# Kernel tuning notes

Measured on AMD Instinct MI355X. Metric: run time of the kernel, lower is better.

## Reference

```python
import jax, jax.numpy as jnp
import numpy as np
from jax import lax

H = 8       # heads == channel dim for conv projections
D = 64      # base_dim (per-head width)
B = 8
N = 1024
EPS = 1e-5  # BatchNorm eps (torch default)


def _bn2d(y, g, b, m, v):
    # inference-mode BatchNorm2d over channel axis 1
    inv = g / jnp.sqrt(v + EPS)
    return (y - m[None, :, None, None]) * inv[None, :, None, None] + b[None, :, None, None]


def _sepconv(xh, dw, dwb, g, bb, m, v, pw, pwb):
    # xh: [b, H, n, d] treated as NCHW; depthwise 3x3 (groups=H) + BN + pointwise 1x1
    y = lax.conv_general_dilated(xh, dw, window_strides=(1, 1),
                                 padding=((1, 1), (1, 1)),
                                 feature_group_count=H,
                                 dimension_numbers=('NCHW', 'OIHW', 'NCHW'))
    y = y + dwb[None, :, None, None]
    y = _bn2d(y, g, bb, m, v)
    # pointwise 1x1 conv == channel mix
    y = jnp.einsum('oc,bchw->bohw', pw[:, :, 0, 0], y) + pwb[None, :, None, None]
    return y


def setup_inputs() -> dict:
    key = jax.random.key(0)
    ks = jax.random.split(key, 12)
    s = 0.1
    x = jax.random.normal(ks[0], (B, N, H * D), jnp.float32)
    dw_w = jax.random.normal(ks[1], (3, H, 1, 3, 3), jnp.float32) * s
    dw_b = jax.random.normal(ks[2], (3, H), jnp.float32) * s
    bn_g = 1.0 + 0.1 * jax.random.normal(ks[3], (3, H), jnp.float32)
    bn_b = jax.random.normal(ks[4], (3, H), jnp.float32) * s
    bn_m = jnp.zeros((3, H), jnp.float32)
    bn_v = jnp.ones((3, H), jnp.float32)
    pw_w = jax.random.normal(ks[5], (3, H, H, 1, 1), jnp.float32) * s
    pw_b = jax.random.normal(ks[6], (3, H), jnp.float32) * s
    re_w = jax.random.normal(ks[7], (H, H, 1, 1), jnp.float32) * 0.3
    re_b = jax.random.normal(ks[8], (H,), jnp.float32) * s
    vn_g = 1.0 + 0.1 * jax.random.normal(ks[9], (H,), jnp.float32)
    vn_b = jax.random.normal(ks[10], (H,), jnp.float32) * s
    vn_m = jnp.zeros((H,), jnp.float32)
    vn_v = jnp.ones((H,), jnp.float32)
    out_w = jax.random.normal(ks[11], (H * D, H * D), jnp.float32) * 0.02
    out_b = jnp.zeros((H * D,), jnp.float32)
    return {"x": x, "dw_w": dw_w, "dw_b": dw_b, "bn_g": bn_g, "bn_b": bn_b,
            "bn_m": bn_m, "bn_v": bn_v, "pw_w": pw_w, "pw_b": pw_b,
            "re_w": re_w, "re_b": re_b, "vn_g": vn_g, "vn_b": vn_b,
            "vn_m": vn_m, "vn_v": vn_v, "out_w": out_w, "out_b": out_b}


def reference(x, dw_w, dw_b, bn_g, bn_b, bn_m, bn_v, pw_w, pw_b,
              re_w, re_b, vn_g, vn_b, vn_m, vn_v, out_w, out_b):
    b, n, hd = x.shape
    d = hd // H
    xh = x.reshape(b, n, H, d).transpose(0, 2, 1, 3)  # [b, h, n, d]
    q, k, v = [
        _sepconv(xh, dw_w[i], dw_b[i], bn_g[i], bn_b[i], bn_m[i], bn_v[i],
                 pw_w[i], pw_b[i])
        for i in range(3)
    ]
    scale = H ** -0.5  # note: original uses dim=heads for scale
    dots = jnp.einsum('bhid,bhjd->bhij', q, k) * scale  # [b,h,n,n]
    attn = jax.nn.softmax(dots, axis=-1)
    # re-attention: 1x1 cross-head conv + BatchNorm (reatten_scale = 1.0)
    attn = jnp.einsum('oc,bcij->boij', re_w[:, :, 0, 0], attn) + re_b[None, :, None, None]
    attn = _bn2d(attn, vn_g, vn_b, vn_m, vn_v)
    out = jnp.einsum('bhij,bhjd->bhid', attn, v)
    out = out.transpose(0, 2, 1, 3).reshape(b, n, hd)
    return out @ out_w.T + out_b
```

## Files before the change

### kernel.cpp

```cpp
#include <hip/hip_runtime.h>


#define EPS 1e-5f
#define SCALE 0.35355339059327373f

typedef float f32x4 __attribute__((ext_vector_type(4)));
typedef short short8 __attribute__((ext_vector_type(8)));
typedef unsigned short ushort;

#define MFMA16(a, b, c) __builtin_amdgcn_mfma_f32_16x16x32_bf16(a, b, c, 0, 0, 0)

__device__ __forceinline__ unsigned short f2bf(float f) {
  union { float f; unsigned u; } v; v.f = f;
  return (unsigned short)((v.u + 0x7FFFu + ((v.u >> 16) & 1u)) >> 16);
}
__device__ __forceinline__ float bf2f(unsigned short h) {
  union { unsigned u; float f; } v; v.u = ((unsigned)h) << 16;
  return v.f;
}
__device__ __forceinline__ int cvtpk(float lo, float hi) {
  int r;
  asm("v_cvt_pk_bf16_f32 %0, %1, %2" : "=v"(r) : "v"(lo), "v"(hi));
  return r;
}

__global__ __launch_bounds__(256) void kprep(
    const float* __restrict__ dwb, const float* __restrict__ bng,
    const float* __restrict__ bnb, const float* __restrict__ bnm,
    const float* __restrict__ bnv, const float* __restrict__ pww,
    const float* __restrict__ pwb, const float* __restrict__ rew,
    const float* __restrict__ reb, const float* __restrict__ vng,
    const float* __restrict__ vnb, const float* __restrict__ vnm,
    const float* __restrict__ vnv, const float* __restrict__ outw,
    float* __restrict__ smalls, float* __restrict__ vsum,
    ushort* __restrict__ wh, ushort* __restrict__ wl) {
  int g = blockIdx.x * 256 + threadIdx.x;
  if (g < 262144) {
    float v = outw[g];
    ushort hi = f2bf(v);
    wh[g] = hi;
    wl[g] = f2bf(v - bf2f(hi));
  }
  if (blockIdx.x >= 1 && blockIdx.x <= 16)
    vsum[(blockIdx.x - 1) * 256 + threadIdx.x] = 0.f;
  if (blockIdx.x == 0) {
    int t = threadIdx.x;
    if (t < 64) {
      int o = t >> 3, c = t & 7;
      float s = vng[o] * rsqrtf(vnv[o] + EPS);
      smalls[t] = rew[o * 8 + c] * s;
    }
    if (t < 8) {
      float s = vng[t] * rsqrtf(vnv[t] + EPS);
      smalls[64 + t] = (reb[t] - vnm[t]) * s + vnb[t];
    }
    if (t < 192) {
      int p = t >> 6, rem = t & 63, o = rem >> 3, c = rem & 7;
      float s = bng[p * 8 + c] * rsqrtf(bnv[p * 8 + c] + EPS);
      smalls[72 + t] = pww[(p * 8 + o) * 8 + c] * s;
    }
    if (t < 24) {
      int p = t / 8, o = t & 7;
      float acc = pwb[p * 8 + o];
      for (int c = 0; c < 8; ++c) {
        float s = bng[p * 8 + c] * rsqrtf(bnv[p * 8 + c] + EPS);
        acc += pww[(p * 8 + o) * 8 + c] *
               ((dwb[p * 8 + c] - bnm[p * 8 + c]) * s + bnb[p * 8 + c]);
      }
      smalls[264 + t] = acc;
    }
  }
}

__global__ __launch_bounds__(256) void kqkv(
    const float* __restrict__ x, const float* __restrict__ dww,
    const float* __restrict__ smalls,
    ushort* __restrict__ qb, ushort* __restrict__ kb,
    float* __restrict__ vf) {
  int t = threadIdx.x;
  int blk = blockIdx.x;
  int b = blk >> 8;
  int n0 = (blk & 255) << 2;
  int d = t & 63;
  int n = n0 + (t >> 6);
  const float* pw_eff = smalls + 72;
  const float* pwb_eff = smalls + 264;
  float y[3][8];
  for (int h = 0; h < 8; ++h) {
    float nb[3][3];
#pragma unroll
    for (int ky = 0; ky < 3; ++ky) {
      int nn = n - 1 + ky;
      bool vr = (nn >= 0) && (nn < 1024);
      const float* xp = x + ((b * 1024 + nn) * 512 + h * 64 + d);
      nb[ky][0] = (vr && d > 0) ? xp[-1] : 0.f;
      nb[ky][1] = vr ? xp[0] : 0.f;
      nb[ky][2] = (vr && d < 63) ? xp[1] : 0.f;
    }
#pragma unroll
    for (int p = 0; p < 3; ++p) {
      const float* w = dww + (p * 8 + h) * 9;
      float a = 0.f;
#pragma unroll
      for (int ky = 0; ky < 3; ++ky)
#pragma unroll
        for (int kx = 0; kx < 3; ++kx) a += w[ky * 3 + kx] * nb[ky][kx];
      y[p][h] = a;
    }
  }
#pragma unroll
  for (int p = 0; p < 3; ++p) {
#pragma unroll
    for (int o = 0; o < 8; ++o) {
      float a = pwb_eff[p * 8 + o];
#pragma unroll
      for (int c = 0; c < 8; ++c) a += pw_eff[p * 64 + o * 8 + c] * y[p][c];
      int idx = ((b * 8 + o) * 1024 + n) * 64 + d;
      if (p == 0) qb[idx] = f2bf(a * SCALE);
      else if (p == 1) kb[idx] = f2bf(a);
      else vf[idx] = a;
    }
  }
}

__global__ __launch_bounds__(256) void kvtrans(const float* __restrict__ vf,
                                               ushort* __restrict__ vt,
                                               float* __restrict__ vsum) {
  __shared__ ushort lds[64 * 65];
  __shared__ float red[256];
  int bh = blockIdx.x >> 4;
  int nt = blockIdx.x & 15;
  int t = threadIdx.x;
  const float* src = vf + (bh * 1024 + nt * 64) * 64;
  float part = 0.f;
#pragma unroll
  for (int it = 0; it < 16; ++it) {
    int nn = (t >> 6) + it * 4;
    int d = t & 63;
    float v = src[nn * 64 + d];
    part += v;
    lds[nn * 65 + d] = f2bf(v);
  }
  red[t] = part;
  __syncthreads();
  ushort* dst = vt + bh * 64 * 1024 + nt * 64;
#pragma unroll
  for (int it = 0; it < 16; ++it) {
    int d = (t >> 6) + it * 4;
    int n = t & 63;
    dst[d * 1024 + n] = lds[n * 65 + d];
  }
  if (t < 64)
    atomicAdd(&vsum[bh * 64 + t],
              red[t] + red[64 + t] + red[128 + t] + red[192 + t]);
}

__global__ __launch_bounds__(512, 4) void kattn(
    const ushort* __restrict__ qb, const ushort* __restrict__ kb,
    const ushort* __restrict__ vt, const float* __restrict__ smalls,
    const float* __restrict__ vsum,
    ushort* __restrict__ ohi, ushort* __restrict__ olo) {
  __shared__ ushort plds[16 * 512];
  __shared__ ushort mlds[8 * 1024];
  int b = blockIdx.x & 7;
  int it = blockIdx.x >> 3;
  int i0 = it * 16;
  int tid = threadIdx.x;
  int w = tid >> 6;
  int l = tid & 63;
  int lrow = l & 15, lgrp = l >> 4;

  const ushort* qh = qb + ((b * 8 + w) * 1024 + i0) * 64;
  const ushort* kh = kb + (b * 8 + w) * 1024 * 64;
  const ushort* vth = vt + (b * 8 + w) * 64 * 1024;

  short8 Qf[2];
#pragma unroll
  for (int kc = 0; kc < 2; ++kc)
    Qf[kc] = *(const short8*)(qh + lrow * 64 + kc * 32 + lgrp * 8);

  int ip = w + ((l >> 5) << 3);
  int jp = (l & 31) << 1;
  int s0 = w >> 2;
  bool s1 = (l >> 5) & 1;

  float Wc[64];
#pragma unroll
  for (int z = 0; z < 64; ++z) {
    int idx = z ^ (s0 << 1);
    Wc[z] = __builtin_bit_cast(
        float, __builtin_amdgcn_readfirstlane(
                   __builtin_bit_cast(int, smalls[idx])));
  }

  float rs[4] = {0.f, 0.f, 0.f, 0.f};
  for (int jt = 0; jt < 16; ++jt) {
    const ushort* kbase = kh + jt * 64 * 64;
    f32x4 acc[4] = {};
#pragma unroll
    for (int q = 0; q < 4; ++q)
#pragma unroll
      for (int kc = 0; kc < 2; ++kc) {
        short8 Kf = *(const short8*)(kbase + (q * 16 + lrow) * 64 + kc * 32 + lgrp * 8);
        acc[q] = MFMA16(Qf[kc], Kf, acc[q]);
      }
#pragma unroll
    for (int q = 0; q < 4; ++q)
#pragma unroll
      for (int r = 0; r < 4; ++r) rs[r] += __expf(acc[q][r]);
  }
#pragma unroll
  for (int r = 0; r < 4; ++r) {
    float v = rs[r];
    v += __shfl_xor(v, 1);
    v += __shfl_xor(v, 2);
    v += __shfl_xor(v, 4);
    v += __shfl_xor(v, 8);
    rs[r] = 1.f / v;
  }

  f32x4 Oacc[4] = {};
  for (int jt = 0; jt < 16; ++jt) {
    const ushort* kbase = kh + jt * 64 * 64;
    f32x4 acc[4] = {};
#pragma unroll
    for (int q = 0; q < 4; ++q)
#pragma unroll
      for (int kc = 0; kc < 2; ++kc) {
        short8 Kf = *(const short8*)(kbase + (q * 16 + lrow) * 64 + kc * 32 + lgrp * 8);
        acc[q] = MFMA16(Qf[kc], Kf, acc[q]);
      }
#pragma unroll
    for (int q = 0; q < 4; ++q)
#pragma unroll
      for (int r = 0; r < 4; ++r) {
        float p = __expf(acc[q][r]) * rs[r];
        int pi = (((lgrp * 4 + r) << 9) + ((q * 16 + lrow) << 3) + w) ^ (lgrp << 1);
        plds[pi] = (ushort)cvtpk(p, p);
      }
    __syncthreads();
    int pbase = (ip << 9) + (jp << 3);
    int4 r0 = *(const int4*)&plds[pbase];
    int4 r1 = *(const int4*)&plds[pbase + 8];
    int e0[4], e1[4];
    e0[0] = s1 ? r0.z : r0.x;  e0[1] = s1 ? r0.w : r0.y;
    e0[2] = s1 ? r0.x : r0.z;  e0[3] = s1 ? r0.y : r0.w;
    e1[0] = s1 ? r1.z : r1.x;  e1[1] = s1 ? r1.w : r1.y;
    e1[2] = s1 ? r1.x : r1.z;  e1[3] = s1 ? r1.y : r1.w;
    float o0[8] = {}, o1[8] = {};
#pragma unroll
    for (int m = 0; m < 4; ++m) {
      float p0l = __builtin_bit_cast(float, e0[m] << 16);
      float p0h = __builtin_bit_cast(float, (unsigned)e0[m] & 0xffff0000u);
      float p1l = __builtin_bit_cast(float, e1[m] << 16);
      float p1h = __builtin_bit_cast(float, (unsigned)e1[m] & 0xffff0000u);
#pragma unroll
      for (int o = 0; o < 8; ++o) {
        o0[o] += Wc[o * 8 + 2 * m] * p0l + Wc[o * 8 + 2 * m + 1] * p0h;
        o1[o] += Wc[o * 8 + 2 * m] * p1l + Wc[o * 8 + 2 * m + 1] * p1h;
      }
    }
#pragma unroll
    for (int o = 0; o < 8; ++o) {
      int pk = cvtpk(o0[o], o1[o]);
      int mi = ((o << 10) + (ip << 6) + jp) ^ ((ip & 7) << 3);
      *(int*)&mlds[mi] = pk;
    }
    __syncthreads();
    short8 PA[2];
#pragma unroll
    for (int kc = 0; kc < 2; ++kc) {
      int ai = ((w << 10) + (lrow << 6) + kc * 32 + lgrp * 8) ^ ((lrow & 7) << 3);
      PA[kc] = *(const short8*)&mlds[ai];
    }
#pragma unroll
    for (int nq = 0; nq < 4; ++nq)
#pragma unroll
      for (int kc = 0; kc < 2; ++kc) {
        short8 Vf = *(const short8*)(vth + (nq * 16 + lrow) * 1024 + jt * 64 + kc * 32 + lgrp * 8);
        Oacc[nq] = MFMA16(PA[kc], Vf, Oacc[nq]);
      }
  }

  float beta = smalls[64 + w];
#pragma unroll
  for (int nq = 0; nq < 4; ++nq)
#pragma unroll
    for (int r = 0; r < 4; ++r) {
      int i = i0 + lgrp * 4 + r;
      int dd = nq * 16 + lrow;
      float o = Oacc[nq][r] + beta * vsum[(b * 8 + w) * 64 + dd];
      int idx = (b * 1024 + i) * 512 + w * 64 + dd;
      ushort hi = (ushort)cvtpk(o, o);
      ohi[idx] = hi;
      olo[idx] = f2bf(o - bf2f(hi));
    }
}

__global__ __launch_bounds__(256) void kout(
    const ushort* __restrict__ ohi, const ushort* __restrict__ olo,
    const ushort* __restrict__ wh, const ushort* __restrict__ wl,
    const float* __restrict__ outb, float* __restrict__ out) {
  int w = threadIdx.x >> 6, l = threadIdx.x & 63;
  int lrow = l & 15, lgrp = l >> 4;
  int i0 = blockIdx.x * 128 + w * 32;
  int n0 = blockIdx.y * 64;
  f32x4 acc[2][4] = {};
  for (int kc = 0; kc < 16; ++kc) {
    short8 Ah[2], Al[2], Bh[4], Bl[4];
#pragma unroll
    for (int a = 0; a < 2; ++a) {
      int ro = (i0 + a * 16 + lrow) * 512 + kc * 32 + lgrp * 8;
      Ah[a] = *(const short8*)(ohi + ro);
      Al[a] = *(const short8*)(olo + ro);
    }
#pragma unroll
    for (int nq = 0; nq < 4; ++nq) {
      int ro = (n0 + nq * 16 + lrow) * 512 + kc * 32 + lgrp * 8;
      Bh[nq] = *(const short8*)(wh + ro);
      Bl[nq] = *(const short8*)(wl + ro);
    }
#pragma unroll
    for (int a = 0; a < 2; ++a)
#pragma unroll
      for (int nq = 0; nq < 4; ++nq) {
        acc[a][nq] = MFMA16(Ah[a], Bh[nq], acc[a][nq]);
        acc[a][nq] = MFMA16(Ah[a], Bl[nq], acc[a][nq]);
        acc[a][nq] = MFMA16(Al[a], Bh[nq], acc[a][nq]);
      }
  }
#pragma unroll
  for (int a = 0; a < 2; ++a)
#pragma unroll
    for (int nq = 0; nq < 4; ++nq)
#pragma unroll
      for (int r = 0; r < 4; ++r) {
        int row = i0 + a * 16 + lgrp * 4 + r;
        int n = n0 + nq * 16 + lrow;
        out[row * 512 + n] = acc[a][nq][r] + outb[n];
      }
}

extern "C" void kernel_launch(void* const* d_in, const int* in_sizes, int n_in,
                              void* d_out, int out_size, void* d_ws, size_t ws_size,
                              hipStream_t stream) {
  const float* x   = (const float*)d_in[0];
  const float* dww = (const float*)d_in[1];
  const float* dwb = (const float*)d_in[2];
  const float* bng = (const float*)d_in[3];
  const float* bnb = (const float*)d_in[4];
  const float* bnm = (const float*)d_in[5];
  const float* bnv = (const float*)d_in[6];
  const float* pww = (const float*)d_in[7];
  const float* pwb = (const float*)d_in[8];
  const float* rew = (const float*)d_in[9];
  const float* reb = (const float*)d_in[10];
  const float* vng = (const float*)d_in[11];
  const float* vnb = (const float*)d_in[12];
  const float* vnm = (const float*)d_in[13];
  const float* vnv = (const float*)d_in[14];
  const float* outw = (const float*)d_in[15];
  const float* outb = (const float*)d_in[16];

  char* ws = (char*)d_ws;
  const size_t MB = 1024 * 1024;
  ushort* qb  = (ushort*)(ws);
  ushort* kb  = (ushort*)(ws + 8 * MB);
  ushort* vt  = (ushort*)(ws + 16 * MB);
  float*  vf  = (float*)(ws + 24 * MB);
  ushort* ohi = (ushort*)(ws + 40 * MB);
  ushort* olo = (ushort*)(ws + 48 * MB);
  ushort* wh  = (ushort*)(ws + 56 * MB);
  ushort* wl  = (ushort*)(ws + 56 * MB + 512 * 1024);
  float* smalls = (float*)(ws + 57 * MB);
  float* vsum   = (float*)(ws + 57 * MB + 4096);

  hipLaunchKernelGGL(kprep, dim3(1024), dim3(256), 0, stream,
                     dwb, bng, bnb, bnm, bnv, pww, pwb, rew, reb, vng, vnb,
                     vnm, vnv, outw, smalls, vsum, wh, wl);
  hipLaunchKernelGGL(kqkv, dim3(2048), dim3(256), 0, stream,
                     x, dww, smalls, qb, kb, vf);
  hipLaunchKernelGGL(kvtrans, dim3(1024), dim3(256), 0, stream, vf, vt, vsum);
  hipLaunchKernelGGL(kattn, dim3(512), dim3(512), 0, stream,
                     qb, kb, vt, smalls, vsum, ohi, olo);
  hipLaunchKernelGGL(kout, dim3(64, 8), dim3(256), 0, stream,
                     ohi, olo, wh, wl, outb, (float*)d_out);
}
```

Before: 349.2 us.

## Split softmax row-sum into separate kernel and restructure attention across heads

Moves the softmax denominator pass out of the attention kernel into a new kernel that accumulates row sums of exp2 scores into a global buffer with atomics. Q is prescaled by log2(e) so exp2 can be used. The attention kernel now has each wave handle a slice of keys for all 8 heads, so the cross-head 1x1 mix happens in registers, and the per-wave partial outputs are reduced through shared memory. V is stored as bf16 instead of fp32 before the transpose. Together these remove the duplicated QK^T pass and the two-phase shared-memory shuffle, at the cost of an extra kernel launch, global atomics and a larger per-thread accumulator footprint (8x4 accumulators).

New measurement: 349.3 us. No clear change (+0.0%).

```diff
diff --git a/kernel.cpp b/kernel.cpp
--- a/kernel.cpp
+++ b/kernel.cpp
@@ -2,7 +2,7 @@
 
 
 #define EPS 1e-5f
-#define SCALE 0.35355339059327373f
+#define SCALE2 0.510138584f
 
 typedef float f32x4 __attribute__((ext_vector_type(4)));
 typedef short short8 __attribute__((ext_vector_type(8)));
@@ -33,7 +33,8 @@
     const float* __restrict__ vnb, const float* __restrict__ vnm,
     const float* __restrict__ vnv, const float* __restrict__ outw,
     float* __restrict__ smalls, float* __restrict__ vsum,
-    ushort* __restrict__ wh, ushort* __restrict__ wl) {
+    float* __restrict__ lsum, ushort* __restrict__ wh,
+    ushort* __restrict__ wl) {
   int g = blockIdx.x * 256 + threadIdx.x;
   if (g < 262144) {
     float v = outw[g];
@@ -43,6 +44,8 @@
   }
   if (blockIdx.x >= 1 && blockIdx.x <= 16)
     vsum[(blockIdx.x - 1) * 256 + threadIdx.x] = 0.f;
+  if (blockIdx.x >= 17 && blockIdx.x <= 272)
+    lsum[(blockIdx.x - 17) * 256 + threadIdx.x] = 0.f;
   if (blockIdx.x == 0) {
     int t = threadIdx.x;
     if (t < 64) {
@@ -76,7 +79,7 @@
     const float* __restrict__ x, const float* __restrict__ dww,
     const float* __restrict__ smalls,
     ushort* __restrict__ qb, ushort* __restrict__ kb,
-    float* __restrict__ vf) {
+    ushort* __restrict__ vb) {
   int t = threadIdx.x;
   int blk = blockIdx.x;
   int b = blk >> 8;
@@ -116,14 +119,14 @@
 #pragma unroll
       for (int c = 0; c < 8; ++c) a += pw_eff[p * 64 + o * 8 + c] * y[p][c];
       int idx = ((b * 8 + o) * 1024 + n) * 64 + d;
-      if (p == 0) qb[idx] = f2bf(a * SCALE);
+      if (p == 0) qb[idx] = f2bf(a * SCALE2);
       else if (p == 1) kb[idx] = f2bf(a);
-      else vf[idx] = a;
-    }
-  }
-}
-
-__global__ __launch_bounds__(256) void kvtrans(const float* __restrict__ vf,
+      else vb[idx] = f2bf(a);
+    }
+  }
+}
+
+__global__ __launch_bounds__(256) void kvtrans(const ushort* __restrict__ vb,
                                                ushort* __restrict__ vt,
                                                float* __restrict__ vsum) {
   __shared__ ushort lds[64 * 65];
@@ -131,15 +134,15 @@
   int bh = blockIdx.x >> 4;
   int nt = blockIdx.x & 15;
   int t = threadIdx.x;
-  const float* src = vf + (bh * 1024 + nt * 64) * 64;
+  const ushort* src = vb + (bh * 1024 + nt * 64) * 64;
   float part = 0.f;
 #pragma unroll
   for (int it = 0; it < 16; ++it) {
     int nn = (t >> 6) + it * 4;
     int d = t & 63;
-    float v = src[nn * 64 + d];
-    part += v;
-    lds[nn * 65 + d] = f2bf(v);
+    ushort v = src[nn * 64 + d];
+    part += bf2f(v);
+    lds[nn * 65 + d] = v;
   }
   red[t] = part;
   __syncthreads();
@@ -155,146 +158,165 @@
               red[t] + red[64 + t] + red[128 + t] + red[192 + t]);
 }
 
-__global__ __launch_bounds__(512, 4) void kattn(
+__global__ __launch_bounds__(512) void kl(const ushort* __restrict__ qb,
+                                          const ushort* __restrict__ kb,
+                                          float* __restrict__ lsum) {
+  __shared__ float lacc[1024];
+  int b = blockIdx.x & 7;
+  int c = (blockIdx.x >> 3) & 7;
+  int jq = blockIdx.x >> 6;
+  int tid = threadIdx.x;
+  int w = tid >> 6, l = tid & 63;
+  int lrow = l & 15, lgrp = l >> 4;
+  lacc[tid] = 0.f;
+  lacc[tid + 512] = 0.f;
+  __syncthreads();
+  const ushort* kh = kb + ((b * 8 + c) * 1024 + jq * 256 + w * 32) * 64;
+  short8 Kf[2][2];
+#pragma unroll
+  for (int jf = 0; jf < 2; ++jf)
+#pragma unroll
+    for (int kc = 0; kc < 2; ++kc)
+      Kf[jf][kc] = *(const short8*)(kh + (jf * 16 + lrow) * 64 + kc * 32 + lgrp * 8);
+  const ushort* qh = qb + (b * 8 + c) * 65536;
+  for (int ci = 0; ci < 64; ++ci) {
+    f32x4 a0 = {}, a1 = {};
+#pragma unroll
+    for (int kc = 0; kc < 2; ++kc) {
+      short8 Qf = *(const short8*)(qh + (ci * 16 + lrow) * 64 + kc * 32 + lgrp * 8);
+      a0 = MFMA16(Kf[0][kc], Qf, a0);
+      a1 = MFMA16(Kf[1][kc], Qf, a1);
+    }
+    float s = 0.f;
+#pragma unroll
+    for (int r = 0; r < 4; ++r) s += exp2f(a0[r]) + exp2f(a1[r]);
+    s += __shfl_xor(s, 16);
+    s += __shfl_xor(s, 32);
+    if (lgrp == 0) atomicAdd(&lacc[ci * 16 + lrow], s);
+  }
+  __syncthreads();
+  atomicAdd(&lsum[(b * 8 + c) * 1024 + tid], lacc[tid]);
+  atomicAdd(&lsum[(b * 8 + c) * 1024 + 512 + tid], lacc[512 + tid]);
+}
+
+__global__ __launch_bounds__(512, 2) void kattn2(
     const ushort* __restrict__ qb, const ushort* __restrict__ kb,
     const ushort* __restrict__ vt, const float* __restrict__ smalls,
-    const float* __restrict__ vsum,
+    const float* __restrict__ vsum, const float* __restrict__ lsum,
     ushort* __restrict__ ohi, ushort* __restrict__ olo) {
-  __shared__ ushort plds[16 * 512];
-  __shared__ ushort mlds[8 * 1024];
+  __shared__ ushort qlds[8192];
+  __shared__ ushort scr[8 * 8 * 16 * 32];
   int b = blockIdx.x & 7;
   int it = blockIdx.x >> 3;
   int i0 = it * 16;
   int tid = threadIdx.x;
-  int w = tid >> 6;
-  int l = tid & 63;
+  int w = tid >> 6, l = tid & 63;
   int lrow = l & 15, lgrp = l >> 4;
 
-  const ushort* qh = qb + ((b * 8 + w) * 1024 + i0) * 64;
-  const ushort* kh = kb + (b * 8 + w) * 1024 * 64;
-  const ushort* vth = vt + (b * 8 + w) * 64 * 1024;
-
-  short8 Qf[2];
-#pragma unroll
-  for (int kc = 0; kc < 2; ++kc)
-    Qf[kc] = *(const short8*)(qh + lrow * 64 + kc * 32 + lgrp * 8);
-
-  int ip = w + ((l >> 5) << 3);
-  int jp = (l & 31) << 1;
-  int s0 = w >> 2;
-  bool s1 = (l >> 5) & 1;
+  {
+    int e = tid * 16;
+    int c = e >> 10, i = (e >> 6) & 15, d0 = e & 63;
+    const ushort* src = qb + ((b * 8 + c) * 1024 + i0 + i) * 64 + d0;
+    int sw = (i & 7) << 3;
+    *(short8*)&qlds[c * 1024 + i * 64 + (d0 ^ sw)] = *(const short8*)src;
+    *(short8*)&qlds[c * 1024 + i * 64 + ((d0 + 8) ^ sw)] = *(const short8*)(src + 8);
+  }
+  __syncthreads();
 
   float Wc[64];
 #pragma unroll
-  for (int z = 0; z < 64; ++z) {
-    int idx = z ^ (s0 << 1);
+  for (int z = 0; z < 64; ++z)
     Wc[z] = __builtin_bit_cast(
         float, __builtin_amdgcn_readfirstlane(
-                   __builtin_bit_cast(int, smalls[idx])));
-  }
-
-  float rs[4] = {0.f, 0.f, 0.f, 0.f};
-  for (int jt = 0; jt < 16; ++jt) {
-    const ushort* kbase = kh + jt * 64 * 64;
-    f32x4 acc[4] = {};
-#pragma unroll
-    for (int q = 0; q < 4; ++q)
-#pragma unroll
-      for (int kc = 0; kc < 2; ++kc) {
-        short8 Kf = *(const short8*)(kbase + (q * 16 + lrow) * 64 + kc * 32 + lgrp * 8);
-        acc[q] = MFMA16(Qf[kc], Kf, acc[q]);
-      }
-#pragma unroll
-    for (int q = 0; q < 4; ++q)
-#pragma unroll
-      for (int r = 0; r < 4; ++r) rs[r] += __expf(acc[q][r]);
-  }
-#pragma unroll
-  for (int r = 0; r < 4; ++r) {
-    float v = rs[r];
-    v += __shfl_xor(v, 1);
-    v += __shfl_xor(v, 2);
-    v += __shfl_xor(v, 4);
-    v += __shfl_xor(v, 8);
-    rs[r] = 1.f / v;
-  }
-
-  f32x4 Oacc[4] = {};
-  for (int jt = 0; jt < 16; ++jt) {
-    const ushort* kbase = kh + jt * 64 * 64;
-    f32x4 acc[4] = {};
-#pragma unroll
-    for (int q = 0; q < 4; ++q)
-#pragma unroll
-      for (int kc = 0; kc < 2; ++kc) {
-        short8 Kf = *(const short8*)(kbase + (q * 16 + lrow) * 64 + kc * 32 + lgrp * 8);
-        acc[q] = MFMA16(Qf[kc], Kf, acc[q]);
-      }
-#pragma unroll
-    for (int q = 0; q < 4; ++q)
-#pragma unroll
-      for (int r = 0; r < 4; ++r) {
-        float p = __expf(acc[q][r]) * rs[r];
-        int pi = (((lgrp * 4 + r) << 9) + ((q * 16 + lrow) << 3) + w) ^ (lgrp << 1);
-        plds[pi] = (ushort)cvtpk(p, p);
-      }
+                   __builtin_bit_cast(int, smalls[z])));
+
+  float linv[8];
+#pragma unroll
+  for (int c = 0; c < 8; ++c)
+    linv[c] = 1.0f / lsum[(b * 8 + c) * 1024 + i0 + lrow];
+
+  const ushort* kh = kb + b * 8 * 65536;
+  const ushort* vh = vt + b * 8 * 65536;
+  int qsw = (lrow & 7) << 3;
+  int ssw = (lrow & 3) << 3;
+  int sbase = (w * 8) * 512 + lrow * 32;
+
+  f32x4 Oacc[8][4] = {};
+
+  for (int ch = 0; ch < 4; ++ch) {
+    int jb = w * 128 + ch * 32;
+#pragma unroll
+    for (int sub = 0; sub < 2; ++sub) {
+      int js = jb + sub * 16;
+      float m[8][4];
+#pragma unroll
+      for (int c = 0; c < 8; ++c) {
+        f32x4 acc = {};
+#pragma unroll
+        for (int kc = 0; kc < 2; ++kc) {
+          short8 Kf = *(const short8*)(kh + c * 65536 + (js + lrow) * 64 +
+                                       kc * 32 + lgrp * 8);
+          short8 Qf = *(const short8*)&qlds[c * 1024 + lrow * 64 +
+                                            ((kc * 32 + lgrp * 8) ^ qsw)];
+          acc = MFMA16(Kf, Qf, acc);
+        }
+        float p[4];
+#pragma unroll
+        for (int r = 0; r < 4; ++r) p[r] = exp2f(acc[r]) * linv[c];
+#pragma unroll
+        for (int o = 0; o < 8; ++o)
+#pragma unroll
+          for (int r = 0; r < 4; ++r) {
+            if (c == 0) m[o][r] = Wc[o * 8] * p[r];
+            else        m[o][r] += Wc[o * 8 + c] * p[r];
+          }
+      }
+      int slot = (sub * 16 + lgrp * 4) ^ ssw;
+#pragma unroll
+      for (int o = 0; o < 8; ++o) {
+        int w0 = cvtpk(m[o][0], m[o][1]);
+        int w1 = cvtpk(m[o][2], m[o][3]);
+        *(int2*)&scr[sbase + o * 512 + slot] = (int2){w0, w1};
+      }
+    }
+    int rslot = (lgrp * 8) ^ ssw;
+#pragma unroll
+    for (int o = 0; o < 8; ++o) {
+      short8 Af = *(const short8*)&scr[sbase + o * 512 + rslot];
+#pragma unroll
+      for (int nq = 0; nq < 4; ++nq) {
+        short8 Vf = *(const short8*)(vh + o * 65536 + (nq * 16 + lrow) * 1024 +
+                                     jb + lgrp * 8);
+        Oacc[o][nq] = MFMA16(Af, Vf, Oacc[o][nq]);
+      }
+    }
+  }
+
+  __syncthreads();
+  float* red = (float*)scr;
+#pragma unroll
+  for (int o = 0; o < 8; ++o) {
+#pragma unroll
+    for (int nq = 0; nq < 4; ++nq)
+#pragma unroll
+      for (int r = 0; r < 4; ++r)
+        red[w * 1024 + (lgrp * 4 + r) * 64 + nq * 16 + lrow] = Oacc[o][nq][r];
     __syncthreads();
-    int pbase = (ip << 9) + (jp << 3);
-    int4 r0 = *(const int4*)&plds[pbase];
-    int4 r1 = *(const int4*)&plds[pbase + 8];
-    int e0[4], e1[4];
-    e0[0] = s1 ? r0.z : r0.x;  e0[1] = s1 ? r0.w : r0.y;
-    e0[2] = s1 ? r0.x : r0.z;  e0[3] = s1 ? r0.y : r0.w;
-    e1[0] = s1 ? r1.z : r1.x;  e1[1] = s1 ? r1.w : r1.y;
-    e1[2] = s1 ? r1.x : r1.z;  e1[3] = s1 ? r1.y : r1.w;
-    float o0[8] = {}, o1[8] = {};
-#pragma unroll
-    for (int m = 0; m < 4; ++m) {
-      float p0l = __builtin_bit_cast(float, e0[m] << 16);
-      float p0h = __builtin_bit_cast(float, (unsigned)e0[m] & 0xffff0000u);
-      float p1l = __builtin_bit_cast(float, e1[m] << 16);
-      float p1h = __builtin_bit_cast(float, (unsigned)e1[m] & 0xffff0000u);
-#pragma unroll
-      for (int o = 0; o < 8; ++o) {
-        o0[o] += Wc[o * 8 + 2 * m] * p0l + Wc[o * 8 + 2 * m + 1] * p0h;
-        o1[o] += Wc[o * 8 + 2 * m] * p1l + Wc[o * 8 + 2 * m + 1] * p1h;
-      }
-    }
-#pragma unroll
-    for (int o = 0; o < 8; ++o) {
-      int pk = cvtpk(o0[o], o1[o]);
-      int mi = ((o << 10) + (ip << 6) + jp) ^ ((ip & 7) << 3);
-      *(int*)&mlds[mi] = pk;
+#pragma unroll
+    for (int e = 0; e < 2; ++e) {
+      int pos = tid + e * 512;
+      int i = pos >> 6, d = pos & 63;
+      float s = 0.f;
+#pragma unroll
+      for (int ww = 0; ww < 8; ++ww) s += red[ww * 1024 + pos];
+      s += smalls[64 + o] * vsum[(b * 8 + o) * 64 + d];
+      int idx = (b * 1024 + i0 + i) * 512 + o * 64 + d;
+      ushort hi = f2bf(s);
+      ohi[idx] = hi;
+      olo[idx] = f2bf(s - bf2f(hi));
     }
     __syncthreads();
-    short8 PA[2];
-#pragma unroll
-    for (int kc = 0; kc < 2; ++kc) {
-      int ai = ((w << 10) + (lrow << 6) + kc * 32 + lgrp * 8) ^ ((lrow & 7) << 3);
-      PA[kc] = *(const short8*)&mlds[ai];
-    }
-#pragma unroll
-    for (int nq = 0; nq < 4; ++nq)
-#pragma unroll
-      for (int kc = 0; kc < 2; ++kc) {
-        short8 Vf = *(const short8*)(vth + (nq * 16 + lrow) * 1024 + jt * 64 + kc * 32 + lgrp * 8);
-        Oacc[nq] = MFMA16(PA[kc], Vf, Oacc[nq]);
-      }
-  }
-
-  float beta = smalls[64 + w];
-#pragma unroll
-  for (int nq = 0; nq < 4; ++nq)
-#pragma unroll
-    for (int r = 0; r < 4; ++r) {
-      int i = i0 + lgrp * 4 + r;
-      int dd = nq * 16 + lrow;
-      float o = Oacc[nq][r] + beta * vsum[(b * 8 + w) * 64 + dd];
-      int idx = (b * 1024 + i) * 512 + w * 64 + dd;
-      ushort hi = (ushort)cvtpk(o, o);
-      ohi[idx] = hi;
-      olo[idx] = f2bf(o - bf2f(hi));
-    }
+  }
 }
 
 __global__ __launch_bounds__(256) void kout(
@@ -367,22 +389,24 @@
   ushort* qb  = (ushort*)(ws);
   ushort* kb  = (ushort*)(ws + 8 * MB);
   ushort* vt  = (ushort*)(ws + 16 * MB);
-  float*  vf  = (float*)(ws + 24 * MB);
-  ushort* ohi = (ushort*)(ws + 40 * MB);
-  ushort* olo = (ushort*)(ws + 48 * MB);
-  ushort* wh  = (ushort*)(ws + 56 * MB);
-  ushort* wl  = (ushort*)(ws + 56 * MB + 512 * 1024);
-  float* smalls = (float*)(ws + 57 * MB);
-  float* vsum   = (float*)(ws + 57 * MB + 4096);
+  ushort* vb  = (ushort*)(ws + 24 * MB);
+  ushort* ohi = (ushort*)(ws + 32 * MB);
+  ushort* olo = (ushort*)(ws + 40 * MB);
+  ushort* wh  = (ushort*)(ws + 48 * MB);
+  ushort* wl  = (ushort*)(ws + 48 * MB + 512 * 1024);
+  float* smalls = (float*)(ws + 49 * MB);
+  float* vsum   = (float*)(ws + 49 * MB + 4096);
+  float* lsum   = (float*)(ws + 49 * MB + 8192 + 16384);
 
   hipLaunchKernelGGL(kprep, dim3(1024), dim3(256), 0, stream,
                      dwb, bng, bnb, bnm, bnv, pww, pwb, rew, reb, vng, vnb,
-                     vnm, vnv, outw, smalls, vsum, wh, wl);
+                     vnm, vnv, outw, smalls, vsum, lsum, wh, wl);
   hipLaunchKernelGGL(kqkv, dim3(2048), dim3(256), 0, stream,
-                     x, dww, smalls, qb, kb, vf);
-  hipLaunchKernelGGL(kvtrans, dim3(1024), dim3(256), 0, stream, vf, vt, vsum);
-  hipLaunchKernelGGL(kattn, dim3(512), dim3(512), 0, stream,
-                     qb, kb, vt, smalls, vsum, ohi, olo);
+                     x, dww, smalls, qb, kb, vb);
+  hipLaunchKernelGGL(kvtrans, dim3(1024), dim3(256), 0, stream, vb, vt, vsum);
+  hipLaunchKernelGGL(kl, dim3(256), dim3(512), 0, stream, qb, kb, lsum);
+  hipLaunchKernelGGL(kattn2, dim3(512), dim3(512), 0, stream,
+                     qb, kb, vt, smalls, vsum, lsum, ohi, olo);
   hipLaunchKernelGGL(kout, dim3(64, 8), dim3(256), 0, stream,
                      ohi, olo, wh, wl, outb, (float*)d_out);
 }
```
